# Performance work log

Measured on AMD Instinct MI355X. Metric: run time of the kernel, lower is better.

## Reference

```python
import jax, jax.numpy as jnp
import numpy as np

D = 128      # state_dim
ED = 20      # edge_dim (RBF basis size)
R = 3        # num message/update rounds
G = 3        # gated equivariant blocks
CUT = 5.0    # cutoff
N = 10000    # nodes
E = 160000   # edges
B = 500      # molecules
HRO = 64     # readout hidden


def setup_inputs() -> dict:
    key = jax.random.key(0)
    ks = jax.random.split(key, 40)
    sc = 0.05

    def nrm(k, shape):
        return jax.random.normal(k, shape, dtype=jnp.float32) * sc

    inp = {
        "h": jax.random.normal(ks[0], (N, 5), dtype=jnp.float32),
        "pos": jax.random.normal(ks[1], (N, 3), dtype=jnp.float32),
        "edge_index": jax.random.randint(ks[2], (2, E), 0, N),
        "batch": jnp.sort(jax.random.randint(ks[3], (N,), 0, B)),
        # node embedding Linear(5, D)
        "emb_w": nrm(ks[4], (5, D)), "emb_b": nrm(ks[5], (D,)),
        # per-round message params (stacked over rounds)
        "msg_phi_w1": nrm(ks[6], (R, D, D)), "msg_phi_b1": nrm(ks[7], (R, D)),
        "msg_phi_w2": nrm(ks[8], (R, D, 3 * D)), "msg_phi_b2": nrm(ks[9], (R, 3 * D)),
        "msg_filt_w": nrm(ks[10], (R, ED, 3 * D)), "msg_filt_b": nrm(ks[11], (R, 3 * D)),
        # per-round update params
        "upd_U": nrm(ks[12], (R, D, D)), "upd_V": nrm(ks[13], (R, D, D)),
        "upd_w1": nrm(ks[14], (R, 2 * D, D)), "upd_b1": nrm(ks[15], (R, D)),
        "upd_w2": nrm(ks[16], (R, D, 3 * D)), "upd_b2": nrm(ks[17], (R, 3 * D)),
        # gated equivariant blocks
        "geb_wv1": nrm(ks[18], (G, D, D)), "geb_wv2": nrm(ks[19], (G, D, D)),
        "geb_w1": nrm(ks[20], (G, 2 * D, D)), "geb_b1": nrm(ks[21], (G, D)),
        "geb_w2": nrm(ks[22], (G, D, 2 * D)), "geb_b2": nrm(ks[23], (G, 2 * D)),
        # invariant readout MLP
        "ro_w1": nrm(ks[24], (D, HRO)), "ro_b1": nrm(ks[25], (HRO,)),
        "ro_w2": nrm(ks[26], (HRO, 1)), "ro_b2": nrm(ks[27], (1,)),
    }
    return inp


def _safe_norm(x, axis):
    return jnp.sqrt(jnp.sum(x * x, axis=axis) + 1e-8)


def reference(h, pos, edge_index, batch,
              emb_w, emb_b,
              msg_phi_w1, msg_phi_b1, msg_phi_w2, msg_phi_b2,
              msg_filt_w, msg_filt_b,
              upd_U, upd_V, upd_w1, upd_b1, upd_w2, upd_b2,
              geb_wv1, geb_wv2, geb_w1, geb_b1, geb_w2, geb_b2,
              ro_w1, ro_b1, ro_w2, ro_b2):
    n_nodes = h.shape[0]
    row, col = edge_index[0], edge_index[1]
    # edge vectors: r_ij = pos[col] - pos[row]
    r_ij = pos[col] - pos[row]                                   # [E,3]
    d = jnp.clip(jnp.linalg.norm(r_ij, axis=1, keepdims=True), 1e-6, None)  # [E,1]
    unit = r_ij / d                                              # [E,3]
    # sinc radial basis + cosine cutoff
    freqs = jnp.arange(1, ED + 1, dtype=h.dtype)
    rbf = jnp.sin(freqs * jnp.pi * d / CUT) / d                  # [E,ED]
    fcut = 0.5 * (jnp.cos(jnp.pi * d / CUT) + 1.0) * (d < CUT)   # [E,1]

    s = h @ emb_w + emb_b                                        # [N,D]
    v = jnp.zeros((n_nodes, D, 3), dtype=h.dtype)                # [N,D,3]

    for r in range(R):
        # --- PaiNNMessage ---
        phi = jax.nn.silu(s @ msg_phi_w1[r] + msg_phi_b1[r]) @ msg_phi_w2[r] + msg_phi_b2[r]  # [N,3D]
        filt = (rbf @ msg_filt_w[r] + msg_filt_b[r]) * fcut      # [E,3D]
        x = phi[col] * filt                                      # gather + modulate  [E,3D]
        xs, xvv, xvw = jnp.split(x, 3, axis=-1)                  # each [E,D]
        ds = jax.ops.segment_sum(xs, row, num_segments=n_nodes)  # [N,D]
        dv_e = xvv[:, :, None] * v[col] + xvw[:, :, None] * unit[:, None, :]  # [E,D,3]
        dv = jax.ops.segment_sum(dv_e, row, num_segments=n_nodes)             # [N,D,3]
        s = s + ds
        v = v + dv
        # --- PaiNNUpdate ---
        Uv = jnp.einsum('ndc,de->nec', v, upd_U[r])              # [N,D,3]
        Vv = jnp.einsum('ndc,de->nec', v, upd_V[r])              # [N,D,3]
        Vn = _safe_norm(Vv, axis=-1)                             # [N,D]
        a = jax.nn.silu(jnp.concatenate([s, Vn], axis=-1) @ upd_w1[r] + upd_b1[r]) @ upd_w2[r] + upd_b2[r]
        a_ss, a_sv, a_vv = jnp.split(a, 3, axis=-1)
        s = s + a_ss + a_sv * jnp.sum(Uv * Vv, axis=-1)
        v = v + a_vv[:, :, None] * Uv

    # --- GatedEquivariantBlocks ---
    for g in range(G):
        v1 = jnp.einsum('ndc,de->nec', v, geb_wv1[g])
        v2 = jnp.einsum('ndc,de->nec', v, geb_wv2[g])
        n2 = _safe_norm(v2, axis=-1)                             # [N,D]
        a = jax.nn.silu(jnp.concatenate([s, n2], axis=-1) @ geb_w1[g] + geb_b1[g]) @ geb_w2[g] + geb_b2[g]
        s_new, gate = jnp.split(a, 2, axis=-1)
        s = s_new
        v = gate[:, :, None] * v1

    # --- InvariantReadout + molwise scatter ---
    out = jax.nn.silu(s @ ro_w1 + ro_b1) @ ro_w2 + ro_b2         # [N,1]
    molwise = jax.ops.segment_sum(out, batch, num_segments=B)    # [B,1]
    return molwise.squeeze(-1)
```

## Files before the change

### kernel.cpp

```cpp
#include <hip/hip_runtime.h>

typedef __attribute__((ext_vector_type(4))) float f32x4;
typedef __attribute__((ext_vector_type(8))) short short8;

#define D 128
#define D3 384
#define SLD 256
#define EDIM 20
#define KPAD 32
#define NR 3
#define NG 3
#define CUTOFF 5.0f
#define NNODES 10000
#define NEDGES 160000
#define NMOL 500
#define HROH 64
#define PI_F 3.14159265358979323846f

#define FBIAS 1
#define FSILU 2
#define FBF16O 4
#define FFCUT 8
#define FA1 16

static __device__ __forceinline__ float silu_f(float x) {
    return x / (1.0f + expf(-x));
}

static __device__ __forceinline__ ushort f2bf(float x) {
    uint u = __float_as_uint(x);
    uint r = (u + 0x7fffu + ((u >> 16) & 1u)) >> 16;
    return (ushort)r;
}
static __device__ __forceinline__ float bf2f(ushort h) {
    return __uint_as_float((uint)h << 16);
}

#define TLR 64
#define TLC 64
#define KC 32
#define APAD 40
#define BPAD 36
#define CPAD 68

__global__ __launch_bounds__(256) void gemm_k(
    const float* __restrict__ A, int lda,
    const float* __restrict__ W, int ldw,
    const float* __restrict__ bias, const float* __restrict__ fcut,
    float* __restrict__ C, ushort* __restrict__ Cbf, int ldc,
    int N, int K, int flags)
{
    const int n0 = blockIdx.x * TLR;
    const int m0 = blockIdx.y * TLC;
    __shared__ ushort SM[9728];
    ushort* Ah = SM;
    ushort* Al = SM + 2560;
    ushort* Bh = SM + 5120;
    ushort* Bl = SM + 7424;
    const int tid = threadIdx.x;
    const int arow = tid & 63;
    const int akq = (tid >> 6) * 4;
    const bool aok = (n0 + arow) < N;
    const float* Ar = A + (size_t)(n0 + arow) * lda;
    const int bk = tid >> 4;
    const int bm = (tid & 15) * 4;
    const float* Wp = W + m0 + bm;
    const int lane = tid & 63;
    const int wrow = (tid >> 6) * 16;
    const int fr = lane & 15;
    const int kg = lane >> 4;

    f32x4 acc[4];
    #pragma unroll
    for (int t = 0; t < 4; ++t) acc[t] = (f32x4){0.f, 0.f, 0.f, 0.f};

    for (int k0 = 0; k0 < K; k0 += KC) {
        #pragma unroll
        for (int half = 0; half < 2; ++half) {
            int kk = akq + half * 16;
            float4 v = aok ? *(const float4*)(Ar + k0 + kk)
                           : make_float4(0.f, 0.f, 0.f, 0.f);
            ushort h0 = f2bf(v.x), h1 = f2bf(v.y), h2 = f2bf(v.z), h3 = f2bf(v.w);
            uint2 ph;
            ph.x = (uint)h0 | ((uint)h1 << 16); ph.y = (uint)h2 | ((uint)h3 << 16);
            *(uint2*)(Ah + arow * APAD + kk) = ph;
            if (!(flags & FA1)) {
                ushort l0 = f2bf(v.x - bf2f(h0)), l1 = f2bf(v.y - bf2f(h1));
                ushort l2 = f2bf(v.z - bf2f(h2)), l3 = f2bf(v.w - bf2f(h3));
                uint2 pl;
                pl.x = (uint)l0 | ((uint)l1 << 16); pl.y = (uint)l2 | ((uint)l3 << 16);
                *(uint2*)(Al + arow * APAD + kk) = pl;
            }
        }
        #pragma unroll
        for (int half = 0; half < 2; ++half) {
            int kk = bk + half * 16;
            float4 v = *(const float4*)(Wp + (size_t)(k0 + kk) * ldw);
            float vv[4] = {v.x, v.y, v.z, v.w};
            #pragma unroll
            for (int i = 0; i < 4; ++i) {
                ushort hh = f2bf(vv[i]);
                ushort ll = f2bf(vv[i] - bf2f(hh));
                Bh[(bm + i) * BPAD + kk] = hh;
                Bl[(bm + i) * BPAD + kk] = ll;
            }
        }
        __syncthreads();
        short8 ah = *(const short8*)(Ah + (wrow + fr) * APAD + kg * 8);
        short8 al;
        if (!(flags & FA1)) al = *(const short8*)(Al + (wrow + fr) * APAD + kg * 8);
        #pragma unroll
        for (int t = 0; t < 4; ++t) {
            const ushort* bp = Bh + (t * 16 + fr) * BPAD + kg * 8;
            const ushort* bq = Bl + (t * 16 + fr) * BPAD + kg * 8;
            short8 bh, bl;
            ((uint2*)&bh)[0] = *(const uint2*)bp;
            ((uint2*)&bh)[1] = *(const uint2*)(bp + 4);
            ((uint2*)&bl)[0] = *(const uint2*)bq;
            ((uint2*)&bl)[1] = *(const uint2*)(bq + 4);
            acc[t] = __builtin_amdgcn_mfma_f32_16x16x32_bf16(ah, bh, acc[t], 0, 0, 0);
            if (!(flags & FA1))
                acc[t] = __builtin_amdgcn_mfma_f32_16x16x32_bf16(al, bh, acc[t], 0, 0, 0);
            acc[t] = __builtin_amdgcn_mfma_f32_16x16x32_bf16(ah, bl, acc[t], 0, 0, 0);
        }
        __syncthreads();
    }

    if (flags & FBF16O) {
        float* Cs = (float*)SM;
        #pragma unroll
        for (int t = 0; t < 4; ++t) {
            #pragma unroll
            for (int r = 0; r < 4; ++r) {
                int row = wrow + kg * 4 + r;
                int n = n0 + row;
                int colm = t * 16 + fr;
                float val = 0.f;
                if (n < N) {
                    val = acc[t][r];
                    if (flags & FBIAS) val += bias[m0 + colm];
                    if (flags & FFCUT) val *= fcut[(size_t)n * 4];
                    if (flags & FSILU) val = silu_f(val);
                }
                Cs[row * CPAD + colm] = val;
            }
        }
        __syncthreads();
        #pragma unroll
        for (int it = 0; it < 2; ++it) {
            int chunk = it * 256 + tid;
            int row = chunk >> 3;
            int c8 = (chunk & 7) * 8;
            int n = n0 + row;
            if (n < N) {
                const float* src = Cs + row * CPAD + c8;
                uint4 pk;
                pk.x = (uint)f2bf(src[0]) | ((uint)f2bf(src[1]) << 16);
                pk.y = (uint)f2bf(src[2]) | ((uint)f2bf(src[3]) << 16);
                pk.z = (uint)f2bf(src[4]) | ((uint)f2bf(src[5]) << 16);
                pk.w = (uint)f2bf(src[6]) | ((uint)f2bf(src[7]) << 16);
                *(uint4*)(Cbf + (size_t)n * ldc + m0 + c8) = pk;
            }
        }
    } else {
        #pragma unroll
        for (int t = 0; t < 4; ++t) {
            #pragma unroll
            for (int r = 0; r < 4; ++r) {
                int n = n0 + wrow + kg * 4 + r;
                if (n < N) {
                    int m = m0 + t * 16 + fr;
                    float val = acc[t][r];
                    if (flags & FBIAS) val += bias[m];
                    if (flags & FFCUT) val *= fcut[(size_t)n * 4];
                    if (flags & FSILU) val = silu_f(val);
                    C[(size_t)n * ldc + m] = val;
                }
            }
        }
    }
}

template <bool WITHDOT>
__global__ __launch_bounds__(256) void uvn_k(
    const float* __restrict__ A,
    const float* __restrict__ WU, const float* __restrict__ WV,
    float* __restrict__ Uv,
    float* __restrict__ DOT,
    float* __restrict__ SX, int N)
{
    const int n0 = blockIdx.x * 32;
    const int m0 = blockIdx.y * 64;
    __shared__ ushort Ah[3][32 * APAD], Al[3][32 * APAD];
    __shared__ ushort Bh[2][64 * BPAD], Bl[2][64 * BPAD];
    const int tid = threadIdx.x;
    const int arow = tid & 31;
    const int akq = (tid >> 5) * 4;
    const bool aok = (n0 + arow) < N;
    const float* Ar = A + (size_t)(n0 + arow) * D3;
    const int bk = tid >> 4;
    const int bm = (tid & 15) * 4;
    const int w = tid >> 6;
    const int rt = w & 1;
    const int ch = w >> 1;
    const int lane = tid & 63;
    const int fr = lane & 15;
    const int kg = lane >> 4;

    f32x4 acc[3][2][2];
    #pragma unroll
    for (int c = 0; c < 3; ++c)
        #pragma unroll
        for (int s = 0; s < 2; ++s)
            #pragma unroll
            for (int t = 0; t < 2; ++t) acc[c][s][t] = (f32x4){0.f, 0.f, 0.f, 0.f};

    for (int k0 = 0; k0 < D; k0 += KC) {
        #pragma unroll
        for (int c = 0; c < 3; ++c) {
            float4 v = aok ? *(const float4*)(Ar + c * D + k0 + akq)
                           : make_float4(0.f, 0.f, 0.f, 0.f);
            ushort h0 = f2bf(v.x), h1 = f2bf(v.y), h2 = f2bf(v.z), h3 = f2bf(v.w);
            ushort l0 = f2bf(v.x - bf2f(h0)), l1 = f2bf(v.y - bf2f(h1));
            ushort l2 = f2bf(v.z - bf2f(h2)), l3 = f2bf(v.w - bf2f(h3));
            uint2 ph, pl;
            ph.x = (uint)h0 | ((uint)h1 << 16); ph.y = (uint)h2 | ((uint)h3 << 16);
            pl.x = (uint)l0 | ((uint)l1 << 16); pl.y = (uint)l2 | ((uint)l3 << 16);
            *(uint2*)(&Ah[c][arow * APAD + akq]) = ph;
            *(uint2*)(&Al[c][arow * APAD + akq]) = pl;
        }
        #pragma unroll
        for (int s = 0; s < 2; ++s) {
            const float* W = s ? WV : WU;
            #pragma unroll
            for (int half = 0; half < 2; ++half) {
                int kk = bk + half * 16;
                float4 v = *(const float4*)(W + (size_t)(k0 + kk) * D + m0 + bm);
                float vv[4] = {v.x, v.y, v.z, v.w};
                #pragma unroll
                for (int i = 0; i < 4; ++i) {
                    ushort hh = f2bf(vv[i]);
                    ushort ll = f2bf(vv[i] - bf2f(hh));
                    Bh[s][(bm + i) * BPAD + kk] = hh;
                    Bl[s][(bm + i) * BPAD + kk] = ll;
                }
            }
        }
        __syncthreads();
        short8 ah[3], al[3];
        #pragma unroll
        for (int c = 0; c < 3; ++c) {
            ah[c] = *(const short8*)(&Ah[c][(rt * 16 + fr) * APAD + kg * 8]);
            al[c] = *(const short8*)(&Al[c][(rt * 16 + fr) * APAD + kg * 8]);
        }
        #pragma unroll
        for (int t = 0; t < 2; ++t) {
            #pragma unroll
            for (int s = 0; s < 2; ++s) {
                const ushort* bp = &Bh[s][(ch * 32 + t * 16 + fr) * BPAD + kg * 8];
                const ushort* bq = &Bl[s][(ch * 32 + t * 16 + fr) * BPAD + kg * 8];
                short8 bh, bl;
                ((uint2*)&bh)[0] = *(const uint2*)bp;
                ((uint2*)&bh)[1] = *(const uint2*)(bp + 4);
                ((uint2*)&bl)[0] = *(const uint2*)bq;
                ((uint2*)&bl)[1] = *(const uint2*)(bq + 4);
                #pragma unroll
                for (int c = 0; c < 3; ++c) {
                    acc[c][s][t] = __builtin_amdgcn_mfma_f32_16x16x32_bf16(ah[c], bh, acc[c][s][t], 0, 0, 0);
                    acc[c][s][t] = __builtin_amdgcn_mfma_f32_16x16x32_bf16(al[c], bh, acc[c][s][t], 0, 0, 0);
                    acc[c][s][t] = __builtin_amdgcn_mfma_f32_16x16x32_bf16(ah[c], bl, acc[c][s][t], 0, 0, 0);
                }
            }
        }
        __syncthreads();
    }
    #pragma unroll
    for (int t = 0; t < 2; ++t) {
        #pragma unroll
        for (int r = 0; r < 4; ++r) {
            int n = n0 + rt * 16 + kg * 4 + r;
            if (n < N) {
                int m = m0 + ch * 32 + t * 16 + fr;
                float ux = acc[0][0][t][r], uy = acc[1][0][t][r], uz = acc[2][0][t][r];
                float vx = acc[0][1][t][r], vy = acc[1][1][t][r], vz = acc[2][1][t][r];
                float* up = Uv + (size_t)n * D3 + m;
                up[0]     = ux;
                up[D]     = uy;
                up[2 * D] = uz;
                SX[(size_t)n * SLD + D + m] =
                    sqrtf(fmaf(vx, vx, fmaf(vy, vy, fmaf(vz, vz, 1e-8f))));
                if (WITHDOT)
                    DOT[(size_t)n * D + m] = fmaf(ux, vx, fmaf(uy, vy, uz * vz));
            }
        }
    }
}

__global__ __launch_bounds__(256) void emb_k(
    const float* __restrict__ h, const float* __restrict__ w,
    const float* __restrict__ b, float* __restrict__ s, int total)
{
    int i = blockIdx.x * 256 + threadIdx.x;
    if (i >= total) return;
    int n = i >> 7, d = i & 127;
    float acc = b[d];
    #pragma unroll
    for (int k = 0; k < 5; ++k) acc = fmaf(h[n * 5 + k], w[k * D + d], acc);
    s[(size_t)n * SLD + d] = acc;
}

__global__ __launch_bounds__(256) void wfpad_k(const float* __restrict__ w,
                                               float* __restrict__ wp)
{
    int i = blockIdx.x * 256 + threadIdx.x;
    if (i >= 3 * KPAD * D3) return;
    int r = i / (KPAD * D3);
    int rem = i % (KPAD * D3);
    int k = rem / D3, m = rem % D3;
    wp[i] = (k < EDIM) ? w[((size_t)r * EDIM + k) * D3 + m] : 0.f;
}

__global__ __launch_bounds__(256) void hist_k(const int* __restrict__ ei,
                                              int* __restrict__ cnt, int E)
{
    int e = blockIdx.x * 256 + threadIdx.x;
    if (e < E) atomicAdd(&cnt[ei[e]], 1);
}

__global__ __launch_bounds__(256) void scan_k(const int* __restrict__ cnt,
                                              int* __restrict__ offs, int n)
{
    __shared__ int tmp[256];
    __shared__ int carry;
    if (threadIdx.x == 0) carry = 0;
    __syncthreads();
    for (int base = 0; base < n; base += 256) {
        int i = base + threadIdx.x;
        int v = (i < n) ? cnt[i] : 0;
        tmp[threadIdx.x] = v;
        __syncthreads();
        for (int off = 1; off < 256; off <<= 1) {
            int add = (threadIdx.x >= off) ? tmp[threadIdx.x - off] : 0;
            __syncthreads();
            tmp[threadIdx.x] += add;
            __syncthreads();
        }
        if (i < n) offs[i + 1] = carry + tmp[threadIdx.x];
        __syncthreads();
        if (threadIdx.x == 255) carry += tmp[255];
        __syncthreads();
    }
    if (threadIdx.x == 0) offs[0] = 0;
}

__global__ __launch_bounds__(256) void initnext_k(const int* __restrict__ offs,
                                                  int* __restrict__ next, int n)
{
    int i = blockIdx.x * 256 + threadIdx.x;
    if (i < n) next[i] = offs[i];
}

__global__ __launch_bounds__(256) void edge_pre_k(
    const int* __restrict__ ei, const float* __restrict__ pos,
    int* __restrict__ next, float* __restrict__ rbf_s,
    float* __restrict__ uf_s, int* __restrict__ col_s, int E)
{
    int e = blockIdx.x * 256 + threadIdx.x;
    if (e >= E) return;
    int r = ei[e], c = ei[E + e];
    float dx = pos[c * 3 + 0] - pos[r * 3 + 0];
    float dy = pos[c * 3 + 1] - pos[r * 3 + 1];
    float dz = pos[c * 3 + 2] - pos[r * 3 + 2];
    float dist = sqrtf(dx * dx + dy * dy + dz * dz);
    float d = fmaxf(dist, 1e-6f);
    float inv = 1.0f / d;
    int p = atomicAdd(&next[r], 1);
    col_s[p] = c;
    uf_s[p * 4 + 0] = dx * inv;
    uf_s[p * 4 + 1] = dy * inv;
    uf_s[p * 4 + 2] = dz * inv;
    uf_s[p * 4 + 3] = (d < CUTOFF) ? 0.5f * (cosf(PI_F * d / CUTOFF) + 1.0f) : 0.0f;
    float w = PI_F * d / CUTOFF;
    float* rb = rbf_s + (size_t)p * KPAD;
    #pragma unroll
    for (int k = 1; k <= EDIM; ++k)
        rb[k - 1] = sinf((float)k * w) * inv;
    #pragma unroll
    for (int k = EDIM; k < KPAD; ++k) rb[k] = 0.f;
}

#define MSG_NPB 2
__global__ __launch_bounds__(256) void message_csr_k(
    const int* __restrict__ offs, const int* __restrict__ col_s,
    const ushort* __restrict__ FILT, const float* __restrict__ uf_s,
    const ushort* __restrict__ Pbf, const float* __restrict__ Vold,
    const ushort* __restrict__ VbfOld,
    float* __restrict__ S, float* __restrict__ Vnew,
    ushort* __restrict__ VbfNew, int N)
{
    const int sub = threadIdx.x >> 7;
    const int d = threadIdx.x & 127;

    auto edge = [&](int j, float& ds, float& dvx, float& dvy, float& dvz) {
        const ushort* fp = FILT + (size_t)j * D3;
        float f0 = bf2f(fp[d]);
        float f1 = bf2f(fp[D + d]);
        float f2 = bf2f(fp[2 * D + d]);
        int col = col_s[j];
        float4 u4 = *(const float4*)(uf_s + (size_t)j * 4);
        const ushort* pc = Pbf + (size_t)col * D3;
        const ushort* vc = VbfOld + (size_t)col * D3;
        float xs  = bf2f(pc[d]) * f0;
        float xvv = bf2f(pc[D + d]) * f1;
        float xvw = bf2f(pc[2 * D + d]) * f2;
        ds += xs;
        dvx = fmaf(xvv, bf2f(vc[d]),         fmaf(xvw, u4.x, dvx));
        dvy = fmaf(xvv, bf2f(vc[D + d]),     fmaf(xvw, u4.y, dvy));
        dvz = fmaf(xvv, bf2f(vc[2 * D + d]), fmaf(xvw, u4.z, dvz));
    };

    int n = blockIdx.x * MSG_NPB + sub;
    if (n >= N) return;
    float ds0 = 0.f, dx0 = 0.f, dy0 = 0.f, dz0 = 0.f;
    float ds1 = 0.f, dx1 = 0.f, dy1 = 0.f, dz1 = 0.f;
    const int j0 = offs[n], j1 = offs[n + 1];
    int j = j0;
    for (; j + 2 <= j1; j += 2) {
        edge(j, ds0, dx0, dy0, dz0);
        edge(j + 1, ds1, dx1, dy1, dz1);
    }
    if (j < j1) edge(j, ds0, dx0, dy0, dz0);
    S[(size_t)n * SLD + d] += ds0 + ds1;
    const float* vo = Vold + (size_t)n * D3;
    float* vn = Vnew + (size_t)n * D3;
    ushort* vb = VbfNew + (size_t)n * D3;
    float nx = vo[d] + dx0 + dx1;
    float ny = vo[D + d] + dy0 + dy1;
    float nz = vo[2 * D + d] + dz0 + dz1;
    vn[d] = nx;         vb[d] = f2bf(nx);
    vn[D + d] = ny;     vb[D + d] = f2bf(ny);
    vn[2 * D + d] = nz; vb[2 * D + d] = f2bf(nz);
}

__global__ __launch_bounds__(256) void upd_apply_k(
    const float* __restrict__ U3, const float* __restrict__ DOT,
    const float* __restrict__ P, float* __restrict__ s,
    float* __restrict__ v, ushort* __restrict__ vbf, int total)
{
    int i = blockIdx.x * 256 + threadIdx.x;
    if (i >= total) return;
    int n = i >> 7, d = i & 127;
    const float* u = U3 + (size_t)n * D3;
    float ux = u[d], uy = u[D + d], uz = u[2 * D + d];
    const float* a = P + (size_t)n * D3;
    s[(size_t)n * SLD + d] += a[d] + a[D + d] * DOT[i];
    float avv = a[2 * D + d];
    float* vv = v + (size_t)n * D3;
    ushort* vb = vbf + (size_t)n * D3;
    float nx = fmaf(avv, ux, vv[d]);
    float ny = fmaf(avv, uy, vv[D + d]);
    float nz = fmaf(avv, uz, vv[2 * D + d]);
    vv[d] = nx;         vb[d] = f2bf(nx);
    vv[D + d] = ny;     vb[D + d] = f2bf(ny);
    vv[2 * D + d] = nz; vb[2 * D + d] = f2bf(nz);
}

__global__ __launch_bounds__(256) void geb_apply_k(
    const float* __restrict__ P, const float* __restrict__ U3,
    float* __restrict__ s, float* __restrict__ v, int total)
{
    int i = blockIdx.x * 256 + threadIdx.x;
    if (i >= total) return;
    int n = i >> 7, d = i & 127;
    const float* a = P + (size_t)n * 2 * D;
    s[(size_t)n * SLD + d] = a[d];
    float g = a[D + d];
    const float* u = U3 + (size_t)n * D3;
    float* vv = v + (size_t)n * D3;
    vv[d]         = g * u[d];
    vv[D + d]     = g * u[D + d];
    vv[2 * D + d] = g * u[2 * D + d];
}

__global__ __launch_bounds__(256) void readout_k(
    const float* __restrict__ H2, const float* __restrict__ w2,
    const float* __restrict__ b2, const int* __restrict__ batch,
    float* __restrict__ out, int N)
{
    int n = blockIdx.x * 256 + threadIdx.x;
    if (n >= N) return;
    float acc = b2[0];
    const float* hrow = H2 + (size_t)n * HROH;
    #pragma unroll
    for (int k = 0; k < HROH; ++k) acc = fmaf(hrow[k], w2[k], acc);
    atomicAdd(out + batch[n], acc);
}


static inline void gemm(hipStream_t st, const float* A, int lda,
                        const float* W, int ldw, const float* bias,
                        const float* fcut,
                        float* C, ushort* Cbf, int ldc,
                        int N, int K, int M, int flags)
{
    dim3 g((N + TLR - 1) / TLR, M / TLC, 1);
    hipLaunchKernelGGL(gemm_k, g, dim3(256), 0, st,
                       A, lda, W, ldw, bias, fcut, C, Cbf, ldc, N, K, flags);
}

extern "C" void kernel_launch(void* const* d_in, const int* in_sizes, int n_in,
                              void* d_out, int out_size, void* d_ws, size_t ws_size,
                              hipStream_t stream)
{
    const float* h          = (const float*)d_in[0];
    const float* pos        = (const float*)d_in[1];
    const int*   ei         = (const int*)d_in[2];
    const int*   batch      = (const int*)d_in[3];
    const float* emb_w      = (const float*)d_in[4];
    const float* emb_b      = (const float*)d_in[5];
    const float* msg_phi_w1 = (const float*)d_in[6];
    const float* msg_phi_b1 = (const float*)d_in[7];
    const float* msg_phi_w2 = (const float*)d_in[8];
    const float* msg_phi_b2 = (const float*)d_in[9];
    const float* msg_filt_w = (const float*)d_in[10];
    const float* msg_filt_b = (const float*)d_in[11];
    const float* upd_U      = (const float*)d_in[12];
    const float* upd_V      = (const float*)d_in[13];
    const float* upd_w1     = (const float*)d_in[14];
    const float* upd_b1     = (const float*)d_in[15];
    const float* upd_w2     = (const float*)d_in[16];
    const float* upd_b2     = (const float*)d_in[17];
    const float* geb_wv1    = (const float*)d_in[18];
    const float* geb_wv2    = (const float*)d_in[19];
    const float* geb_w1     = (const float*)d_in[20];
    const float* geb_b1     = (const float*)d_in[21];
    const float* geb_w2     = (const float*)d_in[22];
    const float* geb_b2     = (const float*)d_in[23];
    const float* ro_w1      = (const float*)d_in[24];
    const float* ro_b1      = (const float*)d_in[25];
    const float* ro_w2      = (const float*)d_in[26];
    const float* ro_b2      = (const float*)d_in[27];
    float* out = (float*)d_out;

    const int N = NNODES, E = NEDGES;

    char* p = (char*)d_ws;
    auto carve = [&](size_t bytes) {
        char* r = p;
        p += (bytes + 255) & ~(size_t)255;
        return r;
    };
    float*  SX   = (float*)carve((size_t)N * SLD * 4);
    float*  VA   = (float*)carve((size_t)N * D3 * 4);
    float*  VB   = (float*)carve((size_t)N * D3 * 4);
    float*  P_   = (float*)carve((size_t)N * D3 * 4);
    ushort* Pbf  = (ushort*)P_;
    ushort* VBFa = (ushort*)carve((size_t)N * D3 * 2);
    ushort* VBFb = (ushort*)carve((size_t)N * D3 * 2);
    float*  H    = (float*)carve((size_t)N * D * 4);
    float*  H2   = (float*)carve((size_t)N * D * 4);
    float*  RBFp = (float*)carve((size_t)E * KPAD * 4);
    float*  UFs  = (float*)carve((size_t)E * 4 * 4);
    int*    COLs = (int*)carve((size_t)E * 4);
    int*    offs = (int*)carve((size_t)(N + 1) * 4);
    int*    nxt  = (int*)carve((size_t)N * 4);
    float*  WFP  = (float*)carve((size_t)3 * KPAD * D3 * 4);
    ushort* FILT = (ushort*)carve((size_t)E * D3 * 2);

    hipMemsetAsync(VA, 0, (size_t)N * D3 * 4, stream);
    hipMemsetAsync(VBFa, 0, (size_t)N * D3 * 2, stream);
    hipLaunchKernelGGL(emb_k, dim3((N * D + 255) / 256), dim3(256), 0, stream,
                       h, emb_w, emb_b, SX, N * D);
    hipLaunchKernelGGL(wfpad_k, dim3((3 * KPAD * D3 + 255) / 256), dim3(256), 0,
                       stream, msg_filt_w, WFP);
    hipMemsetAsync(nxt, 0, (size_t)N * 4, stream);
    hipLaunchKernelGGL(hist_k, dim3((E + 255) / 256), dim3(256), 0, stream, ei, nxt, E);
    hipLaunchKernelGGL(scan_k, dim3(1), dim3(256), 0, stream, nxt, offs, N);
    hipLaunchKernelGGL(initnext_k, dim3((N + 255) / 256), dim3(256), 0, stream,
                       offs, nxt, N);
    hipLaunchKernelGGL(edge_pre_k, dim3((E + 255) / 256), dim3(256), 0, stream,
                       ei, pos, nxt, RBFp, UFs, COLs, E);

    float*  Vc = VA;   ushort* VbfC = VBFa;
    float*  Vs = VB;   ushort* VbfS = VBFb;

    for (int r = 0; r < NR; ++r) {
        gemm(stream, RBFp, KPAD, WFP + (size_t)r * KPAD * D3, D3,
             msg_filt_b + (size_t)r * D3, UFs + 3, nullptr, FILT, D3,
             E, KPAD, D3, FBIAS | FFCUT | FBF16O | FA1);
        gemm(stream, SX, SLD, msg_phi_w1 + (size_t)r * D * D, D,
             msg_phi_b1 + (size_t)r * D, nullptr, H, nullptr, D, N, D, D,
             FBIAS | FSILU);
        gemm(stream, H, D, msg_phi_w2 + (size_t)r * D * D3, D3,
             msg_phi_b2 + (size_t)r * D3, nullptr, nullptr, Pbf, D3, N, D, D3,
             FBIAS | FBF16O);
        hipLaunchKernelGGL(message_csr_k, dim3((N + MSG_NPB - 1) / MSG_NPB),
                           dim3(256), 0, stream,
                           offs, COLs, FILT, UFs, Pbf, Vc, VbfC,
                           SX, Vs, VbfS, N);
        { float* t = Vc; Vc = Vs; Vs = t; }
        { ushort* t = VbfC; VbfC = VbfS; VbfS = t; }
        float* Uv = Vs;
        hipLaunchKernelGGL(HIP_KERNEL_NAME(uvn_k<true>),
                           dim3((N + 31) / 32, 2), dim3(256), 0, stream,
                           Vc, upd_U + (size_t)r * D * D,
                           upd_V + (size_t)r * D * D, Uv, H, SX, N);
        gemm(stream, SX, SLD, upd_w1 + (size_t)r * 2 * D * D, D,
             upd_b1 + (size_t)r * D, nullptr, H2, nullptr, D, N, 2 * D, D,
             FBIAS | FSILU);
        gemm(stream, H2, D, upd_w2 + (size_t)r * D * D3, D3,
             upd_b2 + (size_t)r * D3, nullptr, P_, nullptr, D3, N, D, D3, FBIAS);
        hipLaunchKernelGGL(upd_apply_k, dim3((N * D + 255) / 256), dim3(256), 0,
                           stream, Uv, H, P_, SX, Vc, VbfC, N * D);
    }

    for (int g = 0; g < NG; ++g) {
        float* Uv = Vs;
        hipLaunchKernelGGL(HIP_KERNEL_NAME(uvn_k<false>),
                           dim3((N + 31) / 32, 2), dim3(256), 0, stream,
                           Vc, geb_wv1 + (size_t)g * D * D,
                           geb_wv2 + (size_t)g * D * D, Uv, nullptr, SX, N);
        gemm(stream, SX, SLD, geb_w1 + (size_t)g * 2 * D * D, D,
             geb_b1 + (size_t)g * D, nullptr, H2, nullptr, D, N, 2 * D, D,
             FBIAS | FSILU);
        gemm(stream, H2, D, geb_w2 + (size_t)g * D * 2 * D, 2 * D,
             geb_b2 + (size_t)g * 2 * D, nullptr, P_, nullptr, 2 * D, N, D, 2 * D,
             FBIAS);
        hipLaunchKernelGGL(geb_apply_k, dim3((N * D + 255) / 256), dim3(256), 0,
                           stream, P_, Uv, SX, Vc, N * D);
    }

    gemm(stream, SX, SLD, ro_w1, HROH, ro_b1, nullptr, H2, nullptr, HROH,
         N, D, HROH, FBIAS | FSILU);
    hipMemsetAsync(out, 0, (size_t)NMOL * 4, stream);
    hipLaunchKernelGGL(readout_k, dim3((N + 255) / 256), dim3(256), 0, stream,
                       H2, ro_w2, ro_b2, batch, out, N);
}
```

Measured before the change: 988.0 us.

## Fuse edge filter GEMM with phi gather into dedicated per-edge kernel

Replaces the generic split-bf16 filter GEMM with a dedicated filt_k kernel. It computes the full 384-wide RBF filter per 64-edge tile with single bf16 MFMAs, applies bias and cutoff, then multiplies by the gathered phi output of the neighbor and stores the product X in bf16. The message kernel then reads X directly instead of reading both FILT and Pbf per edge, which cuts its random gathers. In exchange, each filt_k block reloads and converts the whole filter weight matrix into shared memory. The gather of phi now happens during the edge pass in filt_k, and the product is rounded to bf16 once more.

```diff
diff --git a/kernel.cpp b/kernel.cpp
--- a/kernel.cpp
+++ b/kernel.cpp
@@ -20,8 +20,6 @@
 #define FBIAS 1
 #define FSILU 2
 #define FBF16O 4
-#define FFCUT 8
-#define FA1 16
 
 static __device__ __forceinline__ float silu_f(float x) {
     return x / (1.0f + expf(-x));
@@ -34,6 +32,9 @@
 }
 static __device__ __forceinline__ float bf2f(ushort h) {
     return __uint_as_float((uint)h << 16);
+}
+static __device__ __forceinline__ uint pack2(float a, float b) {
+    return (uint)f2bf(a) | ((uint)f2bf(b) << 16);
 }
 
 #define TLR 64
@@ -46,7 +47,7 @@
 __global__ __launch_bounds__(256) void gemm_k(
     const float* __restrict__ A, int lda,
     const float* __restrict__ W, int ldw,
-    const float* __restrict__ bias, const float* __restrict__ fcut,
+    const float* __restrict__ bias,
     float* __restrict__ C, ushort* __restrict__ Cbf, int ldc,
     int N, int K, int flags)
 {
@@ -81,16 +82,13 @@
             float4 v = aok ? *(const float4*)(Ar + k0 + kk)
                            : make_float4(0.f, 0.f, 0.f, 0.f);
             ushort h0 = f2bf(v.x), h1 = f2bf(v.y), h2 = f2bf(v.z), h3 = f2bf(v.w);
-            uint2 ph;
+            ushort l0 = f2bf(v.x - bf2f(h0)), l1 = f2bf(v.y - bf2f(h1));
+            ushort l2 = f2bf(v.z - bf2f(h2)), l3 = f2bf(v.w - bf2f(h3));
+            uint2 ph, pl;
             ph.x = (uint)h0 | ((uint)h1 << 16); ph.y = (uint)h2 | ((uint)h3 << 16);
+            pl.x = (uint)l0 | ((uint)l1 << 16); pl.y = (uint)l2 | ((uint)l3 << 16);
             *(uint2*)(Ah + arow * APAD + kk) = ph;
-            if (!(flags & FA1)) {
-                ushort l0 = f2bf(v.x - bf2f(h0)), l1 = f2bf(v.y - bf2f(h1));
-                ushort l2 = f2bf(v.z - bf2f(h2)), l3 = f2bf(v.w - bf2f(h3));
-                uint2 pl;
-                pl.x = (uint)l0 | ((uint)l1 << 16); pl.y = (uint)l2 | ((uint)l3 << 16);
-                *(uint2*)(Al + arow * APAD + kk) = pl;
-            }
+            *(uint2*)(Al + arow * APAD + kk) = pl;
         }
         #pragma unroll
         for (int half = 0; half < 2; ++half) {
@@ -107,8 +105,7 @@
         }
         __syncthreads();
         short8 ah = *(const short8*)(Ah + (wrow + fr) * APAD + kg * 8);
-        short8 al;
-        if (!(flags & FA1)) al = *(const short8*)(Al + (wrow + fr) * APAD + kg * 8);
+        short8 al = *(const short8*)(Al + (wrow + fr) * APAD + kg * 8);
         #pragma unroll
         for (int t = 0; t < 4; ++t) {
             const ushort* bp = Bh + (t * 16 + fr) * BPAD + kg * 8;
@@ -119,8 +116,7 @@
             ((uint2*)&bl)[0] = *(const uint2*)bq;
             ((uint2*)&bl)[1] = *(const uint2*)(bq + 4);
             acc[t] = __builtin_amdgcn_mfma_f32_16x16x32_bf16(ah, bh, acc[t], 0, 0, 0);
-            if (!(flags & FA1))
-                acc[t] = __builtin_amdgcn_mfma_f32_16x16x32_bf16(al, bh, acc[t], 0, 0, 0);
+            acc[t] = __builtin_amdgcn_mfma_f32_16x16x32_bf16(al, bh, acc[t], 0, 0, 0);
             acc[t] = __builtin_amdgcn_mfma_f32_16x16x32_bf16(ah, bl, acc[t], 0, 0, 0);
         }
         __syncthreads();
@@ -139,7 +135,6 @@
                 if (n < N) {
                     val = acc[t][r];
                     if (flags & FBIAS) val += bias[m0 + colm];
-                    if (flags & FFCUT) val *= fcut[(size_t)n * 4];
                     if (flags & FSILU) val = silu_f(val);
                 }
                 Cs[row * CPAD + colm] = val;
@@ -155,10 +150,10 @@
             if (n < N) {
                 const float* src = Cs + row * CPAD + c8;
                 uint4 pk;
-                pk.x = (uint)f2bf(src[0]) | ((uint)f2bf(src[1]) << 16);
-                pk.y = (uint)f2bf(src[2]) | ((uint)f2bf(src[3]) << 16);
-                pk.z = (uint)f2bf(src[4]) | ((uint)f2bf(src[5]) << 16);
-                pk.w = (uint)f2bf(src[6]) | ((uint)f2bf(src[7]) << 16);
+                pk.x = pack2(src[0], src[1]);
+                pk.y = pack2(src[2], src[3]);
+                pk.z = pack2(src[4], src[5]);
+                pk.w = pack2(src[6], src[7]);
                 *(uint4*)(Cbf + (size_t)n * ldc + m0 + c8) = pk;
             }
         }
@@ -172,10 +167,109 @@
                     int m = m0 + t * 16 + fr;
                     float val = acc[t][r];
                     if (flags & FBIAS) val += bias[m];
-                    if (flags & FFCUT) val *= fcut[(size_t)n * 4];
                     if (flags & FSILU) val = silu_f(val);
                     C[(size_t)n * ldc + m] = val;
                 }
+            }
+        }
+    }
+}
+
+__global__ __launch_bounds__(256) void filt_k(
+    const float* __restrict__ RBFp,
+    const float* __restrict__ WFP,
+    const float* __restrict__ bias,
+    const float* __restrict__ uf_s,
+    const int* __restrict__ col_s,
+    const ushort* __restrict__ Pbf,
+    ushort* __restrict__ X, int E)
+{
+    __shared__ ushort Ah[64 * APAD];
+    __shared__ ushort Bs[D3 * BPAD];
+    __shared__ float  Cs[64 * CPAD];
+    __shared__ int    ColS[64];
+    const int tid = threadIdx.x;
+    const int e0 = blockIdx.x * 64;
+    #pragma unroll
+    for (int it = 0; it < 2; ++it) {
+        int chunk = it * 256 + tid;
+        int row = chunk >> 3;
+        int kq = (chunk & 7) * 4;
+        int e = e0 + row;
+        float4 v = (e < E) ? *(const float4*)(RBFp + (size_t)e * KPAD + kq)
+                           : make_float4(0.f, 0.f, 0.f, 0.f);
+        uint2 ph;
+        ph.x = pack2(v.x, v.y);
+        ph.y = pack2(v.z, v.w);
+        *(uint2*)(Ah + row * APAD + kq) = ph;
+    }
+    for (int m = tid; m < D3; m += 256) {
+        #pragma unroll
+        for (int k = 0; k < KPAD; ++k)
+            Bs[m * BPAD + k] = f2bf(WFP[(size_t)k * D3 + m]);
+    }
+    if (tid < 64) {
+        int e = e0 + tid;
+        ColS[tid] = (e < E) ? col_s[e] : 0;
+    }
+    __syncthreads();
+
+    const int lane = tid & 63;
+    const int wrow = (tid >> 6) * 16;
+    const int fr = lane & 15;
+    const int kg = lane >> 4;
+    short8 ah = *(const short8*)(Ah + (wrow + fr) * APAD + kg * 8);
+    f32x4 acc[24];
+    #pragma unroll
+    for (int t = 0; t < 24; ++t) {
+        const ushort* bp = Bs + (t * 16 + fr) * BPAD + kg * 8;
+        short8 bh;
+        ((uint2*)&bh)[0] = *(const uint2*)bp;
+        ((uint2*)&bh)[1] = *(const uint2*)(bp + 4);
+        acc[t] = __builtin_amdgcn_mfma_f32_16x16x32_bf16(
+            ah, bh, (f32x4){0.f, 0.f, 0.f, 0.f}, 0, 0, 0);
+    }
+    float fc[4];
+    #pragma unroll
+    for (int r = 0; r < 4; ++r) {
+        int e = e0 + wrow + kg * 4 + r;
+        fc[r] = (e < E) ? uf_s[(size_t)e * 4 + 3] : 0.f;
+    }
+    for (int ct = 0; ct < 6; ++ct) {
+        __syncthreads();
+        #pragma unroll
+        for (int tt = 0; tt < 4; ++tt) {
+            int t = ct * 4 + tt;
+            int colm = t * 16 + fr;
+            float b = bias[colm];
+            #pragma unroll
+            for (int r = 0; r < 4; ++r) {
+                int row = wrow + kg * 4 + r;
+                Cs[row * CPAD + tt * 16 + fr] = (acc[t][r] + b) * fc[r];
+            }
+        }
+        __syncthreads();
+        #pragma unroll
+        for (int it = 0; it < 2; ++it) {
+            int chunk = it * 256 + tid;
+            int row = chunk >> 3;
+            int c8 = (chunk & 7) * 8;
+            int e = e0 + row;
+            if (e < E) {
+                int mbase = ct * 64 + c8;
+                int col = ColS[row];
+                uint4 pg = *(const uint4*)(Pbf + (size_t)col * D3 + mbase);
+                const float* src = Cs + row * CPAD + c8;
+                uint4 pk;
+                pk.x = pack2(src[0] * bf2f((ushort)(pg.x & 0xffff)),
+                             src[1] * bf2f((ushort)(pg.x >> 16)));
+                pk.y = pack2(src[2] * bf2f((ushort)(pg.y & 0xffff)),
+                             src[3] * bf2f((ushort)(pg.y >> 16)));
+                pk.z = pack2(src[4] * bf2f((ushort)(pg.z & 0xffff)),
+                             src[5] * bf2f((ushort)(pg.z >> 16)));
+                pk.w = pack2(src[6] * bf2f((ushort)(pg.w & 0xffff)),
+                             src[7] * bf2f((ushort)(pg.w >> 16)));
+                *(uint4*)(X + (size_t)e * D3 + mbase) = pk;
             }
         }
     }
@@ -392,9 +486,8 @@
 #define MSG_NPB 2
 __global__ __launch_bounds__(256) void message_csr_k(
     const int* __restrict__ offs, const int* __restrict__ col_s,
-    const ushort* __restrict__ FILT, const float* __restrict__ uf_s,
-    const ushort* __restrict__ Pbf, const float* __restrict__ Vold,
-    const ushort* __restrict__ VbfOld,
+    const ushort* __restrict__ X, const float* __restrict__ uf_s,
+    const float* __restrict__ Vold, const ushort* __restrict__ VbfOld,
     float* __restrict__ S, float* __restrict__ Vnew,
     ushort* __restrict__ VbfNew, int N)
 {
@@ -402,17 +495,13 @@
     const int d = threadIdx.x & 127;
 
     auto edge = [&](int j, float& ds, float& dvx, float& dvy, float& dvz) {
-        const ushort* fp = FILT + (size_t)j * D3;
-        float f0 = bf2f(fp[d]);
-        float f1 = bf2f(fp[D + d]);
-        float f2 = bf2f(fp[2 * D + d]);
+        const ushort* xp = X + (size_t)j * D3;
+        float xs  = bf2f(xp[d]);
+        float xvv = bf2f(xp[D + d]);
+        float xvw = bf2f(xp[2 * D + d]);
         int col = col_s[j];
         float4 u4 = *(const float4*)(uf_s + (size_t)j * 4);
-        const ushort* pc = Pbf + (size_t)col * D3;
         const ushort* vc = VbfOld + (size_t)col * D3;
-        float xs  = bf2f(pc[d]) * f0;
-        float xvv = bf2f(pc[D + d]) * f1;
-        float xvw = bf2f(pc[2 * D + d]) * f2;
         ds += xs;
         dvx = fmaf(xvv, bf2f(vc[d]),         fmaf(xvw, u4.x, dvx));
         dvy = fmaf(xvv, bf2f(vc[D + d]),     fmaf(xvw, u4.y, dvy));
@@ -499,13 +588,12 @@
 
 static inline void gemm(hipStream_t st, const float* A, int lda,
                         const float* W, int ldw, const float* bias,
-                        const float* fcut,
                         float* C, ushort* Cbf, int ldc,
                         int N, int K, int M, int flags)
 {
     dim3 g((N + TLR - 1) / TLR, M / TLC, 1);
     hipLaunchKernelGGL(gemm_k, g, dim3(256), 0, st,
-                       A, lda, W, ldw, bias, fcut, C, Cbf, ldc, N, K, flags);
+                       A, lda, W, ldw, bias, C, Cbf, ldc, N, K, flags);
 }
 
 extern "C" void kernel_launch(void* const* d_in, const int* in_sizes, int n_in,
@@ -565,7 +653,7 @@
     int*    offs = (int*)carve((size_t)(N + 1) * 4);
     int*    nxt  = (int*)carve((size_t)N * 4);
     float*  WFP  = (float*)carve((size_t)3 * KPAD * D3 * 4);
-    ushort* FILT = (ushort*)carve((size_t)E * D3 * 2);
+    ushort* X    = (ushort*)carve((size_t)E * D3 * 2);
 
     hipMemsetAsync(VA, 0, (size_t)N * D3 * 4, stream);
     hipMemsetAsync(VBFa, 0, (size_t)N * D3 * 2, stream);
@@ -585,19 +673,17 @@
     float*  Vs = VB;   ushort* VbfS = VBFb;
 
     for (int r = 0; r < NR; ++r) {
-        gemm(stream, RBFp, KPAD, WFP + (size_t)r * KPAD * D3, D3,
-             msg_filt_b + (size_t)r * D3, UFs + 3, nullptr, FILT, D3,
-             E, KPAD, D3, FBIAS | FFCUT | FBF16O | FA1);
         gemm(stream, SX, SLD, msg_phi_w1 + (size_t)r * D * D, D,
-             msg_phi_b1 + (size_t)r * D, nullptr, H, nullptr, D, N, D, D,
-             FBIAS | FSILU);
+             msg_phi_b1 + (size_t)r * D, H, nullptr, D, N, D, D, FBIAS | FSILU);
         gemm(stream, H, D, msg_phi_w2 + (size_t)r * D * D3, D3,
-             msg_phi_b2 + (size_t)r * D3, nullptr, nullptr, Pbf, D3, N, D, D3,
+             msg_phi_b2 + (size_t)r * D3, nullptr, Pbf, D3, N, D, D3,
              FBIAS | FBF16O);
+        hipLaunchKernelGGL(filt_k, dim3((E + 63) / 64), dim3(256), 0, stream,
+                           RBFp, WFP + (size_t)r * KPAD * D3,
+                           msg_filt_b + (size_t)r * D3, UFs, COLs, Pbf, X, E);
         hipLaunchKernelGGL(message_csr_k, dim3((N + MSG_NPB - 1) / MSG_NPB),
                            dim3(256), 0, stream,
-                           offs, COLs, FILT, UFs, Pbf, Vc, VbfC,
-                           SX, Vs, VbfS, N);
+                           offs, COLs, X, UFs, Vc, VbfC, SX, Vs, VbfS, N);
         { float* t = Vc; Vc = Vs; Vs = t; }
         { ushort* t = VbfC; VbfC = VbfS; VbfS = t; }
         float* Uv = Vs;
@@ -606,10 +692,9 @@
                            Vc, upd_U + (size_t)r * D * D,
                            upd_V + (size_t)r * D * D, Uv, H, SX, N);
         gemm(stream, SX, SLD, upd_w1 + (size_t)r * 2 * D * D, D,
-             upd_b1 + (size_t)r * D, nullptr, H2, nullptr, D, N, 2 * D, D,
-             FBIAS | FSILU);
+             upd_b1 + (size_t)r * D, H2, nullptr, D, N, 2 * D, D, FBIAS | FSILU);
         gemm(stream, H2, D, upd_w2 + (size_t)r * D * D3, D3,
-             upd_b2 + (size_t)r * D3, nullptr, P_, nullptr, D3, N, D, D3, FBIAS);
+             upd_b2 + (size_t)r * D3, P_, nullptr, D3, N, D, D3, FBIAS);
         hipLaunchKernelGGL(upd_apply_k, dim3((N * D + 255) / 256), dim3(256), 0,
                            stream, Uv, H, P_, SX, Vc, VbfC, N * D);
     }
@@ -621,17 +706,15 @@
                            Vc, geb_wv1 + (size_t)g * D * D,
                            geb_wv2 + (size_t)g * D * D, Uv, nullptr, SX, N);
         gemm(stream, SX, SLD, geb_w1 + (size_t)g * 2 * D * D, D,
-             geb_b1 + (size_t)g * D, nullptr, H2, nullptr, D, N, 2 * D, D,
-             FBIAS | FSILU);
+             geb_b1 + (size_t)g * D, H2, nullptr, D, N, 2 * D, D, FBIAS | FSILU);
         gemm(stream, H2, D, geb_w2 + (size_t)g * D * 2 * D, 2 * D,
-             geb_b2 + (size_t)g * 2 * D, nullptr, P_, nullptr, 2 * D, N, D, 2 * D,
-             FBIAS);
+             geb_b2 + (size_t)g * 2 * D, P_, nullptr, 2 * D, N, D, 2 * D, FBIAS);
         hipLaunchKernelGGL(geb_apply_k, dim3((N * D + 255) / 256), dim3(256), 0,
                            stream, P_, Uv, SX, Vc, N * D);
     }
 
-    gemm(stream, SX, SLD, ro_w1, HROH, ro_b1, nullptr, H2, nullptr, HROH,
-         N, D, HROH, FBIAS | FSILU);
+    gemm(stream, SX, SLD, ro_w1, HROH, ro_b1, H2, nullptr, HROH, N, D, HROH,
+         FBIAS | FSILU);
     hipMemsetAsync(out, 0, (size_t)NMOL * 4, stream);
     hipLaunchKernelGGL(readout_k, dim3((N + 255) / 256), dim3(256), 0, stream,
                        H2, ro_w2, ro_b2, batch, out, N);
```

New measurement: 877.3 us. 1.13x faster.
